# Kernel optimization log

Measured on AMD Instinct MI355X. Metric: run time of the kernel, lower is better.

## Reference

```python
import jax, jax.numpy as jnp
import numpy as np

S, B, H = 1024, 4, 1024
NH, NC = 16, 4            # num_attention_heads, num_combined_heads
HPH = H // NH             # 64
NF = NH // NC             # num_FFN = 4
FFM = 8                   # combined_FFN_multiple
DIN = NC * HPH            # 256, grouped FFN input dim
DHID = FFM * DIN          # 2048, dense_in output dim
DH2 = DHID // 2           # 1024, GLU half / dense_out input dim
EPS = 1e-6
NORM_FACTOR = 1.0 / float(np.sqrt(HPH))


def _ln(x, g, b):
    m = x.mean(-1, keepdims=True)
    v = ((x - m) ** 2).mean(-1, keepdims=True)
    return (x - m) * jax.lax.rsqrt(v + EPS) * g + b


def setup_inputs() -> dict:
    key = jax.random.key(0)
    ks = jax.random.split(key, 10)
    p = lambda k, shape: jax.random.normal(k, shape, jnp.float32) * 0.02
    return {
        "hidden_states": jax.random.normal(ks[0], (S, B, H), jnp.float32),
        "g1": jnp.ones((H,), jnp.float32), "b1": jnp.zeros((H,), jnp.float32),
        "g2": jnp.ones((HPH,), jnp.float32), "b2": jnp.zeros((HPH,), jnp.float32),
        "Wq": p(ks[1], (H, H)), "bq": jnp.zeros((H,), jnp.float32),
        "Wk": p(ks[2], (H, H)), "bk": jnp.zeros((H,), jnp.float32),
        "Wv": p(ks[3], (H, H)), "bv": jnp.zeros((H,), jnp.float32),
        "W_in": p(ks[4], (NF, DIN, DHID)), "b_in": jnp.zeros((NF, DHID), jnp.float32),
        "W_out": p(ks[5], (NF, DH2, DIN)), "b_out": jnp.zeros((NF, DIN), jnp.float32),
        "Wd": p(ks[6], (H, H)), "bd": jnp.zeros((H,), jnp.float32),
    }


def reference(hidden_states, g1, b1, g2, b2, Wq, bq, Wk, bk, Wv, bv,
              W_in, b_in, W_out, b_out, Wd, bd):
    # hidden_states: [S, B, H]
    x = _ln(hidden_states, g1, b1)                       # norm1

    def heads(t):  # [S,B,H] -> [B*NH, S, HPH] (matches view + transpose in torch)
        return jnp.transpose(t.reshape(S, B * NH, HPH), (1, 0, 2))

    q = heads(x @ Wq + bq)
    k = heads(x @ Wk + bk)
    v = heads(x @ Wv + bv)

    # subtraction_gaussian_kernel: pairwise squared euclidean distance
    qk = jnp.einsum('nsd,ntd->nst', q, k)                # [B*NH, S, S]
    q2 = jnp.sum(q * q, axis=-1)
    k2 = jnp.sum(k * k, axis=-1)
    dist = q2[:, :, None] + k2[None if False else slice(None), None, :][0] if False else q2[:, :, None] + k2[:, None, :] - 2.0 * qk
    matmul_result = dist * (-0.5 * NORM_FACTOR)          # scores <= 0

    # Exp sequence op: elementwise exp (softmax replacement, no normalization)
    probs = jnp.exp(matmul_result)

    ctx = jnp.einsum('nst,ntd->nsd', probs, v)           # [B*NH, S, HPH]
    ctx = jnp.transpose(ctx, (1, 0, 2)).reshape(S, B, H)
    ctx = x + ctx                                        # residual with norm1 output (as in source)

    ctx = _ln(ctx.reshape(S, B, NH, HPH), g2, b2)        # per-head norm2

    # grouped FFN over contiguous head subsets (vectorized over the NF groups)
    cg = ctx.reshape(S, B, NF, DIN)
    h = jnp.einsum('sbgi,gio->sbgo', cg, W_in) + b_in    # [S,B,NF,DHID]
    xh, yh = jnp.split(h, 2, axis=-1)
    h = xh * jax.nn.relu(yh)                             # GLU-style x * relu(y)
    og = jnp.einsum('sbgi,gio->sbgo', h, W_out) + b_out  # [S,B,NF,DIN]

    out = og.reshape(S, B, H) @ Wd + bd                  # attention_dense
    return out, matmul_result
```

## Files before the change

### kernel.cpp

```cpp
#include <hip/hip_runtime.h>


typedef __attribute__((ext_vector_type(8))) short short8;
typedef __attribute__((ext_vector_type(4))) float f32x4;

__device__ __forceinline__ unsigned short f2bf(float f) {
  union { float f; unsigned u; } x; x.f = f;
  unsigned r = x.u + 0x7FFFu + ((x.u >> 16) & 1u);
  return (unsigned short)(r >> 16);
}
__device__ __forceinline__ float bf2f(unsigned short u) {
  union { float f; unsigned u; } x; x.u = ((unsigned)u) << 16;
  return x.f;
}
__device__ __forceinline__ unsigned cvtpk(float a, float b) {
  unsigned r;
  asm("v_cvt_pk_bf16_f32 %0, %1, %2" : "=v"(r) : "v"(a), "v"(b));
  return r;
}
__device__ __forceinline__ void gload16(const unsigned short* g, unsigned short* l) {
  __builtin_amdgcn_global_load_lds(
      (const __attribute__((address_space(1))) unsigned int*)g,
      (__attribute__((address_space(3))) unsigned int*)l, 16, 0, 0);
}

__global__ __launch_bounds__(256) void ln1_kernel(
    const float* __restrict__ x, const float* __restrict__ g,
    const float* __restrict__ b, float* __restrict__ y,
    unsigned short* __restrict__ ybf)
{
  const long base = (long)blockIdx.x * 1024;
  const int c = threadIdx.x * 4;
  float4 v = *(const float4*)(x + base + c);
  float s = v.x + v.y + v.z + v.w;
  float ss = v.x*v.x + v.y*v.y + v.z*v.z + v.w*v.w;
  #pragma unroll
  for (int off = 32; off > 0; off >>= 1) {
    s  += __shfl_xor(s, off);
    ss += __shfl_xor(ss, off);
  }
  __shared__ float sw[4], ssw[4];
  const int wave = threadIdx.x >> 6;
  if ((threadIdx.x & 63) == 0) { sw[wave] = s; ssw[wave] = ss; }
  __syncthreads();
  s  = sw[0] + sw[1] + sw[2] + sw[3];
  ss = ssw[0] + ssw[1] + ssw[2] + ssw[3];
  const float mean = s * (1.0f/1024.0f);
  const float var  = ss * (1.0f/1024.0f) - mean*mean;
  const float rs   = rsqrtf(var + 1e-6f);
  const float4 gv = *(const float4*)(g + c);
  const float4 bv = *(const float4*)(b + c);
  float4 o;
  o.x = (v.x - mean) * rs * gv.x + bv.x;
  o.y = (v.y - mean) * rs * gv.y + bv.y;
  o.z = (v.z - mean) * rs * gv.z + bv.z;
  o.w = (v.w - mean) * rs * gv.w + bv.w;
  *(float4*)(y + base + c) = o;
  ushort4 ob;
  ob.x = f2bf(o.x); ob.y = f2bf(o.y); ob.z = f2bf(o.z); ob.w = f2bf(o.w);
  *(ushort4*)(ybf + base + c) = ob;
}

__device__ __forceinline__ void transpose_body(
    const float* __restrict__ Wg, unsigned short* __restrict__ WTg,
    int K, int N, int bx, int by, int tid)
{
  __shared__ float T[32][33];
  const int n0 = bx * 32, k0 = by * 32;
  const int r = tid >> 3, c4 = (tid & 7) * 4;
  float4 v = *(const float4*)(Wg + (long)(k0 + r) * N + n0 + c4);
  T[r][c4+0] = v.x; T[r][c4+1] = v.y; T[r][c4+2] = v.z; T[r][c4+3] = v.w;
  __syncthreads();
  ushort4 o;
  o.x = f2bf(T[c4+0][r]); o.y = f2bf(T[c4+1][r]);
  o.z = f2bf(T[c4+2][r]); o.w = f2bf(T[c4+3][r]);
  *(ushort4*)(WTg + (long)(n0 + r) * K + k0 + c4) = o;
}

__global__ __launch_bounds__(256) void prep_weights_kernel(
    const float* __restrict__ Wq, const float* __restrict__ Wk,
    const float* __restrict__ Wv, const float* __restrict__ Wd,
    const float* __restrict__ Win, const float* __restrict__ Wout,
    const float* __restrict__ bq, const float* __restrict__ bk,
    const float* __restrict__ bv,
    unsigned short* __restrict__ wqkvT, unsigned short* __restrict__ wdT,
    unsigned short* __restrict__ winT, unsigned short* __restrict__ woutT,
    float* __restrict__ qkvb)
{
  const int idx = blockIdx.x;
  const int tid = threadIdx.x;
  if (idx < 4096) {
    const int z = idx >> 10, rem = idx & 1023;
    const float* W = (z == 0) ? Wq : (z == 1) ? Wk : (z == 2) ? Wv : Wd;
    unsigned short* WT = (z == 3) ? wdT : wqkvT + (long)z * 1048576;
    transpose_body(W, WT, 1024, 1024, rem & 31, rem >> 5, tid);
  } else if (idx < 6144) {
    const int rem = idx - 4096;
    const int z = rem >> 9, r2 = rem & 511;
    transpose_body(Win + (long)z * 524288, winT + (long)z * 524288,
                   256, 2048, r2 & 63, r2 >> 6, tid);
  } else if (idx < 7168) {
    const int rem = idx - 6144;
    const int z = rem >> 8, r2 = rem & 255;
    transpose_body(Wout + (long)z * 262144, woutT + (long)z * 262144,
                   1024, 256, r2 & 7, r2 >> 3, tid);
  } else {
    const int i = (idx - 7168) * 256 + tid;
    qkvb[i] = (i < 1024) ? bq[i] : ((i < 2048) ? bk[i - 1024] : bv[i - 2048]);
  }
}

__global__ __launch_bounds__(256) void mfma_gemm_kernel(
    const unsigned short* __restrict__ A, int lda, long agoff,
    const unsigned short* __restrict__ BT, long bgoff, int K,
    const float* __restrict__ bias, int biasoff,
    unsigned short* __restrict__ Cbf, float* __restrict__ Cf,
    int ldc, int cgoff)
{
  const int g = blockIdx.z;
  const unsigned short* Ag = A + (long)g * agoff;
  const unsigned short* Bg = BT + (long)g * bgoff;
  const float* biasg = bias + (long)g * biasoff;
  const int row0 = blockIdx.y * 128, col0 = blockIdx.x * 128;
  __shared__ __align__(16) unsigned short As[128 * 64];
  __shared__ __align__(16) unsigned short Bs[128 * 64];
  const int tid = threadIdx.x;
  const int w = tid >> 6, l = tid & 63;
  const int ms = (w & 1) << 6, ns = (w >> 1) << 6;
  const int fr = l & 15, fg = l >> 4;
  const int lr8 = l >> 3, ls8 = l & 7;
  const int scol = (ls8 ^ lr8) << 3;
  const int rsw = fr & 7;
  f32x4 acc[4][4];
  #pragma unroll
  for (int i = 0; i < 4; ++i)
    #pragma unroll
    for (int j = 0; j < 4; ++j) acc[i][j] = (f32x4)0.0f;

  for (int k0 = 0; k0 < K; k0 += 64) {
    #pragma unroll
    for (int g8 = 0; g8 < 4; ++g8) {
      const int r = (w << 5) + (g8 << 3);
      gload16(Ag + (long)(row0 + r + lr8) * lda + k0 + scol, &As[r * 64]);
      gload16(Bg + (long)(col0 + r + lr8) * K  + k0 + scol, &Bs[r * 64]);
    }
    __syncthreads();
    #pragma unroll
    for (int ks = 0; ks < 2; ++ks) {
      const int rslot = (((ks << 2) + fg) ^ rsw) << 3;
      short8 af[4], bfr[4];
      #pragma unroll
      for (int i = 0; i < 4; ++i)
        af[i] = *(const short8*)&As[(ms + i*16 + fr) * 64 + rslot];
      #pragma unroll
      for (int j = 0; j < 4; ++j)
        bfr[j] = *(const short8*)&Bs[(ns + j*16 + fr) * 64 + rslot];
      #pragma unroll
      for (int i = 0; i < 4; ++i)
        #pragma unroll
        for (int j = 0; j < 4; ++j)
          acc[i][j] = __builtin_amdgcn_mfma_f32_16x16x32_bf16(bfr[j], af[i], acc[i][j], 0, 0, 0);
    }
    __syncthreads();
  }

  #pragma unroll
  for (int j = 0; j < 4; ++j) {
    const float4 bj4 = *(const float4*)(biasg + col0 + ns + j*16 + (fg << 2));
    #pragma unroll
    for (int i = 0; i < 4; ++i) {
      const long row = row0 + ms + i*16 + fr;
      const long cb = row * ldc + (long)g * cgoff + col0 + ns + j*16 + (fg << 2);
      const float v0 = acc[i][j][0] + bj4.x, v1 = acc[i][j][1] + bj4.y;
      const float v2 = acc[i][j][2] + bj4.z, v3 = acc[i][j][3] + bj4.w;
      if (Cbf) {
        uint2 pk; pk.x = cvtpk(v0, v1); pk.y = cvtpk(v2, v3);
        *(uint2*)(Cbf + cb) = pk;
      } else {
        f32x4 o = {v0, v1, v2, v3};
        __builtin_nontemporal_store(o, (f32x4*)(Cf + cb));
      }
    }
  }
}

__global__ __launch_bounds__(256) void mfma_gemm64_kernel(
    const unsigned short* __restrict__ A, int lda, long agoff,
    const unsigned short* __restrict__ BT, long bgoff, int K,
    const float* __restrict__ bias, int biasoff,
    unsigned short* __restrict__ Cbf, float* __restrict__ Cf,
    int ldc, int cgoff)
{
  const int g = blockIdx.z;
  const unsigned short* Ag = A + (long)g * agoff;
  const unsigned short* Bg = BT + (long)g * bgoff;
  const float* biasg = bias + (long)g * biasoff;
  const int row0 = blockIdx.y * 128, col0 = blockIdx.x * 64;
  __shared__ __align__(16) unsigned short As[128 * 64];
  __shared__ __align__(16) unsigned short Bs[64 * 64];
  const int tid = threadIdx.x;
  const int w = tid >> 6, l = tid & 63;
  const int ms = (w & 1) << 6, ns = (w >> 1) << 5;
  const int fr = l & 15, fg = l >> 4;
  const int lr8 = l >> 3, ls8 = l & 7;
  const int scol = (ls8 ^ lr8) << 3;
  const int rsw = fr & 7;
  f32x4 acc[4][2];
  #pragma unroll
  for (int i = 0; i < 4; ++i)
    #pragma unroll
    for (int j = 0; j < 2; ++j) acc[i][j] = (f32x4)0.0f;

  for (int k0 = 0; k0 < K; k0 += 64) {
    #pragma unroll
    for (int g8 = 0; g8 < 4; ++g8) {
      const int r = (w << 5) + (g8 << 3);
      gload16(Ag + (long)(row0 + r + lr8) * lda + k0 + scol, &As[r * 64]);
    }
    #pragma unroll
    for (int g8 = 0; g8 < 2; ++g8) {
      const int r = (w << 4) + (g8 << 3);
      gload16(Bg + (long)(col0 + r + lr8) * K + k0 + scol, &Bs[r * 64]);
    }
    __syncthreads();
    #pragma unroll
    for (int ks = 0; ks < 2; ++ks) {
      const int rslot = (((ks << 2) + fg) ^ rsw) << 3;
      short8 af[4], bfr[2];
      #pragma unroll
      for (int i = 0; i < 4; ++i)
        af[i] = *(const short8*)&As[(ms + i*16 + fr) * 64 + rslot];
      #pragma unroll
      for (int j = 0; j < 2; ++j)
        bfr[j] = *(const short8*)&Bs[(ns + j*16 + fr) * 64 + rslot];
      #pragma unroll
      for (int i = 0; i < 4; ++i)
        #pragma unroll
        for (int j = 0; j < 2; ++j)
          acc[i][j] = __builtin_amdgcn_mfma_f32_16x16x32_bf16(bfr[j], af[i], acc[i][j], 0, 0, 0);
    }
    __syncthreads();
  }

  #pragma unroll
  for (int j = 0; j < 2; ++j) {
    const float4 bj4 = *(const float4*)(biasg + col0 + ns + j*16 + (fg << 2));
    #pragma unroll
    for (int i = 0; i < 4; ++i) {
      const long row = row0 + ms + i*16 + fr;
      const long cb = row * ldc + (long)g * cgoff + col0 + ns + j*16 + (fg << 2);
      const float v0 = acc[i][j][0] + bj4.x, v1 = acc[i][j][1] + bj4.y;
      const float v2 = acc[i][j][2] + bj4.z, v3 = acc[i][j][3] + bj4.w;
      if (Cbf) {
        uint2 pk; pk.x = cvtpk(v0, v1); pk.y = cvtpk(v2, v3);
        *(uint2*)(Cbf + cb) = pk;
      } else {
        f32x4 o = {v0, v1, v2, v3};
        __builtin_nontemporal_store(o, (f32x4*)(Cf + cb));
      }
    }
  }
}

__global__ __launch_bounds__(256) void mfma_glu_kernel(
    const unsigned short* __restrict__ A,
    const unsigned short* __restrict__ WT,
    const float* __restrict__ bin,
    unsigned short* __restrict__ H2)
{
  const int g = blockIdx.z;
  const unsigned short* Ag = A + g * 256;
  const unsigned short* Wg = WT + (long)g * 2048 * 256;
  const float* bg = bin + g * 2048;
  const int row0 = blockIdx.y * 128, col0 = blockIdx.x * 64;
  __shared__ __align__(16) unsigned short As[128 * 64];
  __shared__ __align__(16) unsigned short Bxs[64 * 64];
  __shared__ __align__(16) unsigned short Bys[64 * 64];
  const int tid = threadIdx.x;
  const int w = tid >> 6, l = tid & 63;
  const int ms = (w & 1) << 6, ns = (w >> 1) << 5;
  const int fr = l & 15, fg = l >> 4;
  const int lr8 = l >> 3, ls8 = l & 7;
  const int scol = (ls8 ^ lr8) << 3;
  const int rsw = fr & 7;
  f32x4 ax[4][2], ay[4][2];
  #pragma unroll
  for (int i = 0; i < 4; ++i)
    #pragma unroll
    for (int j = 0; j < 2; ++j) { ax[i][j] = (f32x4)0.0f; ay[i][j] = (f32x4)0.0f; }

  for (int k0 = 0; k0 < 256; k0 += 64) {
    #pragma unroll
    for (int g8 = 0; g8 < 4; ++g8) {
      const int r = (w << 5) + (g8 << 3);
      gload16(Ag + (long)(row0 + r + lr8) * 1024 + k0 + scol, &As[r * 64]);
    }
    #pragma unroll
    for (int g8 = 0; g8 < 2; ++g8) {
      const int r = (w << 4) + (g8 << 3);
      gload16(Wg + (long)(col0 + r + lr8) * 256 + k0 + scol,          &Bxs[r * 64]);
      gload16(Wg + (long)(1024 + col0 + r + lr8) * 256 + k0 + scol,   &Bys[r * 64]);
    }
    __syncthreads();
    #pragma unroll
    for (int ks = 0; ks < 2; ++ks) {
      const int rslot = (((ks << 2) + fg) ^ rsw) << 3;
      short8 af[4], bx[2], by[2];
      #pragma unroll
      for (int i = 0; i < 4; ++i)
        af[i] = *(const short8*)&As[(ms + i*16 + fr) * 64 + rslot];
      #pragma unroll
      for (int j = 0; j < 2; ++j) {
        bx[j] = *(const short8*)&Bxs[(ns + j*16 + fr) * 64 + rslot];
        by[j] = *(const short8*)&Bys[(ns + j*16 + fr) * 64 + rslot];
      }
      #pragma unroll
      for (int i = 0; i < 4; ++i)
        #pragma unroll
        for (int j = 0; j < 2; ++j) {
          ax[i][j] = __builtin_amdgcn_mfma_f32_16x16x32_bf16(bx[j], af[i], ax[i][j], 0, 0, 0);
          ay[i][j] = __builtin_amdgcn_mfma_f32_16x16x32_bf16(by[j], af[i], ay[i][j], 0, 0, 0);
        }
    }
    __syncthreads();
  }

  #pragma unroll
  for (int j = 0; j < 2; ++j) {
    const float4 bx4 = *(const float4*)(bg + col0 + ns + j*16 + (fg << 2));
    const float4 by4 = *(const float4*)(bg + 1024 + col0 + ns + j*16 + (fg << 2));
    #pragma unroll
    for (int i = 0; i < 4; ++i) {
      const long row = row0 + ms + i*16 + fr;
      const long cb = row * 4096 + g * 1024 + col0 + ns + j*16 + (fg << 2);
      float o4[4];
      const float* bxp = &bx4.x; const float* byp = &by4.x;
      #pragma unroll
      for (int r4 = 0; r4 < 4; ++r4) {
        const float xh = ax[i][j][r4] + bxp[r4];
        const float yh = ay[i][j][r4] + byp[r4];
        o4[r4] = xh * fmaxf(yh, 0.0f);
      }
      uint2 pk; pk.x = cvtpk(o4[0], o4[1]); pk.y = cvtpk(o4[2], o4[3]);
      *(uint2*)(H2 + cb) = pk;
    }
  }
}

__global__ __launch_bounds__(256) void prep_attn_kernel(
    const unsigned short* __restrict__ qkv,
    float* __restrict__ q2g, float* __restrict__ k2g,
    unsigned short* __restrict__ vt)
{
  const int n = blockIdx.y, s0 = blockIdx.x * 64;
  const int b = n >> 4, hoff = (n & 15) * 64;
  const int tid = threadIdx.x;
  __shared__ unsigned short T[64][72];
  #pragma unroll
  for (int p = 0; p < 2; ++p) {
    const int r = (tid >> 3) + p * 32, c = (tid & 7) << 3;
    *(short8*)&T[r][c] = *(const short8*)(qkv + ((long)((s0 + r) * 4 + b)) * 3072 + 2048 + hoff + c);
  }
  {
    const int r = tid >> 2, e = tid & 3;
    const long base = ((long)((s0 + r) * 4 + b)) * 3072 + hoff + (e << 4);
    float sq = 0.f, sk = 0.f;
    #pragma unroll
    for (int ch = 0; ch < 2; ++ch) {
      short8 q8 = *(const short8*)(qkv + base + (ch << 3));
      short8 k8 = *(const short8*)(qkv + base + 1024 + (ch << 3));
      #pragma unroll
      for (int ee = 0; ee < 8; ++ee) {
        float f = bf2f((unsigned short)q8[ee]); sq = fmaf(f, f, sq);
        f = bf2f((unsigned short)k8[ee]); sk = fmaf(f, f, sk);
      }
    }
    sq += __shfl_xor(sq, 1); sq += __shfl_xor(sq, 2);
    sk += __shfl_xor(sk, 1); sk += __shfl_xor(sk, 2);
    if (e == 0) {
      q2g[n * 1024 + s0 + r] = sq;
      k2g[n * 1024 + s0 + r] = sk;
    }
  }
  __syncthreads();
  #pragma unroll
  for (int p = 0; p < 2; ++p) {
    const int d = (tid >> 3) + p * 32, sc = (tid & 7) << 3;
    short8 o;
    #pragma unroll
    for (int j = 0; j < 8; ++j) o[j] = (short)T[sc + j][d];
    *(short8*)(vt + ((long)n * 64 + d) * 1024 + s0 + sc) = o;
  }
}

__global__ __launch_bounds__(256) void attn_kernel(
    const unsigned short* __restrict__ qkv, const unsigned short* __restrict__ vt,
    const float* __restrict__ q2g, const float* __restrict__ k2g,
    const float* __restrict__ xln, const float* __restrict__ g2,
    const float* __restrict__ b2,
    unsigned short* __restrict__ ctx2, float* __restrict__ scores)
{
  const int n = blockIdx.y;
  const int s0 = blockIdx.x * 64;
  const int b = n >> 4, hoff = (n & 15) * 64;
  __shared__ __align__(16) unsigned short Qs[64][72];
  __shared__ __align__(16) unsigned short Ks[2][64 * 64];
  __shared__ __align__(16) unsigned short VTl[2][64 * 64];
  __shared__ __align__(16) unsigned short Ps[64][72];
  const int tid = threadIdx.x, w = tid >> 6, l = tid & 63;
  const int fr = l & 15, fg = l >> 4;
  const int lr8 = l >> 3, ls8 = l & 7;
  const int sslot = ((ls8 ^ lr8) << 3);
  const int rsw = fr & 7;

  #pragma unroll
  for (int p = 0; p < 2; ++p) {
    const int r = (tid >> 3) + p * 32, c = (tid & 7) << 3;
    *(short8*)&Qs[r][c] = *(const short8*)(qkv + ((long)((s0 + r) * 4 + b)) * 3072 + hoff + c);
  }
  float q2m[4];
  #pragma unroll
  for (int i = 0; i < 4; ++i) q2m[i] = -0.0625f * q2g[n * 1024 + s0 + i*16 + fr];

  #pragma unroll
  for (int p = 0; p < 2; ++p) {
    const int rowb = p * 32 + w * 8;
    gload16(qkv + ((long)((rowb + lr8) * 4 + b)) * 3072 + 1024 + hoff + sslot, &Ks[0][rowb * 64]);
    gload16(vt + ((long)n * 64 + rowb + lr8) * 1024 + sslot,                   &VTl[0][rowb * 64]);
  }
  __syncthreads();

  f32x4 o[4];
  #pragma unroll
  for (int i = 0; i < 4; ++i) o[i] = (f32x4)0.0f;

  int cur = 0;
  for (int t0 = 0; t0 < 1024; t0 += 64) {
    if (t0 + 64 < 1024) {
      #pragma unroll
      for (int p = 0; p < 2; ++p) {
        const int rowb = p * 32 + w * 8;
        gload16(qkv + ((long)((t0 + 64 + rowb + lr8) * 4 + b)) * 3072 + 1024 + hoff + sslot,
                &Ks[cur ^ 1][rowb * 64]);
        gload16(vt + ((long)n * 64 + rowb + lr8) * 1024 + t0 + 64 + sslot,
                &VTl[cur ^ 1][rowb * 64]);
      }
    }
    const float4 k2v4 = *(const float4*)(k2g + n * 1024 + t0 + (w << 4) + (fg << 2));
    const float k2m[4] = {-0.0625f*k2v4.x, -0.0625f*k2v4.y, -0.0625f*k2v4.z, -0.0625f*k2v4.w};

    f32x4 c4[4];
    #pragma unroll
    for (int i = 0; i < 4; ++i) c4[i] = (f32x4)0.0f;
    #pragma unroll
    for (int ks = 0; ks < 2; ++ks) {
      const short8 kf = *(const short8*)&Ks[cur][((w << 4) + fr) * 64 + ((((ks << 2) + fg) ^ rsw) << 3)];
      #pragma unroll
      for (int i = 0; i < 4; ++i) {
        const short8 qf = *(const short8*)&Qs[i*16 + fr][(ks << 5) + (fg << 3)];
        c4[i] = __builtin_amdgcn_mfma_f32_16x16x32_bf16(kf, qf, c4[i], 0, 0, 0);
      }
    }
    #pragma unroll
    for (int i = 0; i < 4; ++i) {
      f32x4 sc;
      float pe[4];
      #pragma unroll
      for (int r4 = 0; r4 < 4; ++r4) {
        const float m = fmaf(c4[i][r4], 0.125f, q2m[i] + k2m[r4]);
        sc[r4] = m;
        pe[r4] = __expf(m);
      }
      __builtin_nontemporal_store(sc,
          (f32x4*)(scores + (long)n * 1048576 + (long)(s0 + i*16 + fr) * 1024 + t0 + (w << 4) + (fg << 2)));
      uint2 pk; pk.x = cvtpk(pe[0], pe[1]); pk.y = cvtpk(pe[2], pe[3]);
      *(uint2*)&Ps[i*16 + fr][(w << 4) + (fg << 2)] = pk;
    }
    __syncthreads();

    #pragma unroll
    for (int ks = 0; ks < 2; ++ks) {
      const short8 vb = *(const short8*)&VTl[cur][((w << 4) + fr) * 64 + ((((ks << 2) + fg) ^ rsw) << 3)];
      #pragma unroll
      for (int i = 0; i < 4; ++i) {
        const short8 pf = *(const short8*)&Ps[i*16 + fr][(ks << 5) + (fg << 3)];
        o[i] = __builtin_amdgcn_mfma_f32_16x16x32_bf16(vb, pf, o[i], 0, 0, 0);
      }
    }
    __syncthreads();
    cur ^= 1;
  }

  const int dbase = (w << 4) + (fg << 2);
  float4 xl4[4];
  #pragma unroll
  for (int i = 0; i < 4; ++i)
    xl4[i] = *(const float4*)(xln + ((long)((s0 + i*16 + fr) * 4 + b)) * 1024 + hoff + dbase);

  float* redbuf = (float*)&Ps[0][0];
  const int slot = (w << 2) + fg;
  #pragma unroll
  for (int i = 0; i < 4; ++i) {
    float s = 0.f, ss = 0.f;
    const float* xp = &xl4[i].x;
    #pragma unroll
    for (int r4 = 0; r4 < 4; ++r4) {
      const float v = o[i][r4] + xp[r4];
      s += v; ss = fmaf(v, v, ss);
    }
    redbuf[(i*16 + fr) * 16 + slot] = s;
    redbuf[1024 + (i*16 + fr) * 16 + slot] = ss;
  }
  __syncthreads();
  float* statbuf = (float*)&Qs[0][0];
  {
    const int row = tid >> 2, q4 = tid & 3;
    float s = 0.f, ss = 0.f;
    #pragma unroll
    for (int k = 0; k < 4; ++k) {
      s  += redbuf[row * 16 + q4 * 4 + k];
      ss += redbuf[1024 + row * 16 + q4 * 4 + k];
    }
    s  += __shfl_xor(s, 1);  s  += __shfl_xor(s, 2);
    ss += __shfl_xor(ss, 1); ss += __shfl_xor(ss, 2);
    if (q4 == 0) {
      const float mean = s * (1.0f/64.0f);
      const float var  = ss * (1.0f/64.0f) - mean * mean;
      statbuf[row] = mean;
      statbuf[64 + row] = rsqrtf(var + 1e-6f);
    }
  }
  __syncthreads();
  const float4 g2v = *(const float4*)(g2 + dbase);
  const float4 b2v = *(const float4*)(b2 + dbase);
  const float* gp = &g2v.x; const float* bp = &b2v.x;
  #pragma unroll
  for (int i = 0; i < 4; ++i) {
    const float mean = statbuf[i*16 + fr];
    const float rs   = statbuf[64 + i*16 + fr];
    const float* xp = &xl4[i].x;
    float vo[4];
    #pragma unroll
    for (int r4 = 0; r4 < 4; ++r4)
      vo[r4] = (o[i][r4] + xp[r4] - mean) * rs * gp[r4] + bp[r4];
    uint2 pk; pk.x = cvtpk(vo[0], vo[1]); pk.y = cvtpk(vo[2], vo[3]);
    *(uint2*)(ctx2 + ((long)((s0 + i*16 + fr) * 4 + b)) * 1024 + hoff + dbase) = pk;
  }
}

extern "C" void kernel_launch(void* const* d_in, const int* in_sizes, int n_in,
                              void* d_out, int out_size, void* d_ws, size_t ws_size,
                              hipStream_t stream) {
  const float* hs   = (const float*)d_in[0];
  const float* g1   = (const float*)d_in[1];
  const float* b1   = (const float*)d_in[2];
  const float* g2   = (const float*)d_in[3];
  const float* b2   = (const float*)d_in[4];
  const float* Wq   = (const float*)d_in[5];
  const float* bq   = (const float*)d_in[6];
  const float* Wk   = (const float*)d_in[7];
  const float* bk   = (const float*)d_in[8];
  const float* Wv   = (const float*)d_in[9];
  const float* bv   = (const float*)d_in[10];
  const float* Win  = (const float*)d_in[11];
  const float* bin  = (const float*)d_in[12];
  const float* Wout = (const float*)d_in[13];
  const float* bout = (const float*)d_in[14];
  const float* Wd   = (const float*)d_in[15];
  const float* bd   = (const float*)d_in[16];

  char* ws = (char*)d_ws;
  float*          xln   = (float*)(ws + 0);
  unsigned short* xbf   = (unsigned short*)(ws + 16777216);
  unsigned short* qkv   = (unsigned short*)(ws + 25165824);
  unsigned short* ctx2  = (unsigned short*)(ws + 67108864);
  unsigned short* wqkvT = (unsigned short*)(ws + 75497472);
  unsigned short* winT  = (unsigned short*)(ws + 81788928);
  unsigned short* woutT = (unsigned short*)(ws + 85983232);
  unsigned short* wdT   = (unsigned short*)(ws + 88080384);
  float*          qkvb  = (float*)(ws + 90177536);
  unsigned short* vt    = (unsigned short*)(ws + 90189824);
  float*          q2g   = (float*)(ws + 98578432);
  float*          k2g   = (float*)(ws + 98840576);
  unsigned short* h2    = (unsigned short*)(ws + 16777216);
  unsigned short* og    = (unsigned short*)(ws + 0);

  float* out0 = (float*)d_out;
  float* out1 = out0 + 4194304;

  ln1_kernel<<<4096, 256, 0, stream>>>(hs, g1, b1, xln, xbf);

  prep_weights_kernel<<<7180, 256, 0, stream>>>(
      Wq, Wk, Wv, Wd, Win, Wout, bq, bk, bv, wqkvT, wdT, winT, woutT, qkvb);

  mfma_gemm_kernel<<<dim3(24,32,1), 256, 0, stream>>>(
      xbf, 1024, 0, wqkvT, 0, 1024, qkvb, 0, qkv, nullptr, 3072, 0);

  prep_attn_kernel<<<dim3(16,64), 256, 0, stream>>>(qkv, q2g, k2g, vt);

  attn_kernel<<<dim3(16,64), 256, 0, stream>>>(qkv, vt, q2g, k2g, xln, g2, b2, ctx2, out1);

  mfma_glu_kernel<<<dim3(16,32,4), 256, 0, stream>>>(ctx2, winT, bin, h2);

  mfma_gemm64_kernel<<<dim3(4,32,4), 256, 0, stream>>>(
      h2, 4096, 1024, woutT, 262144, 1024, bout, 256, og, nullptr, 1024, 256);

  mfma_gemm64_kernel<<<dim3(16,32,1), 256, 0, stream>>>(
      og, 1024, 0, wdT, 0, 1024, bd, 0, nullptr, out0, 1024, 0);
}
```

Baseline: 246.5 us.

## Double-buffer LDS tiles with async prefetch in MFMA GEMM kernels

The three MFMA GEMM kernels (generic 128x128, 128x64, and GLU) now keep two LDS stages. Global-to-LDS loads for tile t+2 are issued right after the fragments of tile t have been read into registers, with explicit vmcnt waits, barriers and raised priority around the MFMA block. This is meant to overlap global memory latency with matrix compute instead of stalling on every K step. In exchange it doubles LDS use, which may lower occupancy, and it relies on hand-counted vmcnt values that must match the number of loads in flight.

```diff
diff --git a/kernel.cpp b/kernel.cpp
--- a/kernel.cpp
+++ b/kernel.cpp
@@ -122,8 +122,8 @@
   const unsigned short* Bg = BT + (long)g * bgoff;
   const float* biasg = bias + (long)g * biasoff;
   const int row0 = blockIdx.y * 128, col0 = blockIdx.x * 128;
-  __shared__ __align__(16) unsigned short As[128 * 64];
-  __shared__ __align__(16) unsigned short Bs[128 * 64];
+  __shared__ __align__(16) unsigned short As[2][128 * 64];
+  __shared__ __align__(16) unsigned short Bs[2][128 * 64];
   const int tid = threadIdx.x;
   const int w = tid >> 6, l = tid & 63;
   const int ms = (w & 1) << 6, ns = (w >> 1) << 6;
@@ -137,31 +137,55 @@
     #pragma unroll
     for (int j = 0; j < 4; ++j) acc[i][j] = (f32x4)0.0f;
 
-  for (int k0 = 0; k0 < K; k0 += 64) {
+  const int nt = K >> 6;
+  #pragma unroll
+  for (int sidx = 0; sidx < 2; ++sidx) {
+    const int k0 = sidx << 6;
     #pragma unroll
     for (int g8 = 0; g8 < 4; ++g8) {
       const int r = (w << 5) + (g8 << 3);
-      gload16(Ag + (long)(row0 + r + lr8) * lda + k0 + scol, &As[r * 64]);
-      gload16(Bg + (long)(col0 + r + lr8) * K  + k0 + scol, &Bs[r * 64]);
-    }
-    __syncthreads();
+      gload16(Ag + (long)(row0 + r + lr8) * lda + k0 + scol, &As[sidx][r * 64]);
+      gload16(Bg + (long)(col0 + r + lr8) * K  + k0 + scol, &Bs[sidx][r * 64]);
+    }
+  }
+  int cur = 0;
+  for (int t = 0; t < nt; ++t) {
+    if (t + 1 < nt) asm volatile("s_waitcnt vmcnt(8)" ::: "memory");
+    else            asm volatile("s_waitcnt vmcnt(0)" ::: "memory");
+    __builtin_amdgcn_s_barrier();
+    __builtin_amdgcn_sched_barrier(0);
+    short8 af[2][4], bfr[2][4];
     #pragma unroll
     for (int ks = 0; ks < 2; ++ks) {
       const int rslot = (((ks << 2) + fg) ^ rsw) << 3;
-      short8 af[4], bfr[4];
-      #pragma unroll
-      for (int i = 0; i < 4; ++i)
-        af[i] = *(const short8*)&As[(ms + i*16 + fr) * 64 + rslot];
-      #pragma unroll
-      for (int j = 0; j < 4; ++j)
-        bfr[j] = *(const short8*)&Bs[(ns + j*16 + fr) * 64 + rslot];
+      #pragma unroll
+      for (int i = 0; i < 4; ++i) {
+        af[ks][i]  = *(const short8*)&As[cur][(ms + i*16 + fr) * 64 + rslot];
+        bfr[ks][i] = *(const short8*)&Bs[cur][(ns + i*16 + fr) * 64 + rslot];
+      }
+    }
+    asm volatile("s_waitcnt lgkmcnt(0)" ::: "memory");
+    __builtin_amdgcn_sched_barrier(0);
+    __builtin_amdgcn_s_barrier();
+    if (t + 2 < nt) {
+      const int k0 = (t + 2) << 6;
+      #pragma unroll
+      for (int g8 = 0; g8 < 4; ++g8) {
+        const int r = (w << 5) + (g8 << 3);
+        gload16(Ag + (long)(row0 + r + lr8) * lda + k0 + scol, &As[cur][r * 64]);
+        gload16(Bg + (long)(col0 + r + lr8) * K  + k0 + scol, &Bs[cur][r * 64]);
+      }
+    }
+    __builtin_amdgcn_s_setprio(1);
+    #pragma unroll
+    for (int ks = 0; ks < 2; ++ks)
       #pragma unroll
       for (int i = 0; i < 4; ++i)
         #pragma unroll
         for (int j = 0; j < 4; ++j)
-          acc[i][j] = __builtin_amdgcn_mfma_f32_16x16x32_bf16(bfr[j], af[i], acc[i][j], 0, 0, 0);
-    }
-    __syncthreads();
+          acc[i][j] = __builtin_amdgcn_mfma_f32_16x16x32_bf16(bfr[ks][j], af[ks][i], acc[i][j], 0, 0, 0);
+    __builtin_amdgcn_s_setprio(0);
+    cur ^= 1;
   }
 
   #pragma unroll
@@ -196,8 +220,8 @@
   const unsigned short* Bg = BT + (long)g * bgoff;
   const float* biasg = bias + (long)g * biasoff;
   const int row0 = blockIdx.y * 128, col0 = blockIdx.x * 64;
-  __shared__ __align__(16) unsigned short As[128 * 64];
-  __shared__ __align__(16) unsigned short Bs[64 * 64];
+  __shared__ __align__(16) unsigned short As[2][128 * 64];
+  __shared__ __align__(16) unsigned short Bs[2][64 * 64];
   const int tid = threadIdx.x;
   const int w = tid >> 6, l = tid & 63;
   const int ms = (w & 1) << 6, ns = (w >> 1) << 5;
@@ -211,35 +235,64 @@
     #pragma unroll
     for (int j = 0; j < 2; ++j) acc[i][j] = (f32x4)0.0f;
 
-  for (int k0 = 0; k0 < K; k0 += 64) {
+  const int nt = K >> 6;
+  #pragma unroll
+  for (int sidx = 0; sidx < 2; ++sidx) {
+    const int k0 = sidx << 6;
     #pragma unroll
     for (int g8 = 0; g8 < 4; ++g8) {
       const int r = (w << 5) + (g8 << 3);
-      gload16(Ag + (long)(row0 + r + lr8) * lda + k0 + scol, &As[r * 64]);
+      gload16(Ag + (long)(row0 + r + lr8) * lda + k0 + scol, &As[sidx][r * 64]);
     }
     #pragma unroll
     for (int g8 = 0; g8 < 2; ++g8) {
       const int r = (w << 4) + (g8 << 3);
-      gload16(Bg + (long)(col0 + r + lr8) * K + k0 + scol, &Bs[r * 64]);
-    }
-    __syncthreads();
+      gload16(Bg + (long)(col0 + r + lr8) * K + k0 + scol, &Bs[sidx][r * 64]);
+    }
+  }
+  int cur = 0;
+  for (int t = 0; t < nt; ++t) {
+    if (t + 1 < nt) asm volatile("s_waitcnt vmcnt(6)" ::: "memory");
+    else            asm volatile("s_waitcnt vmcnt(0)" ::: "memory");
+    __builtin_amdgcn_s_barrier();
+    __builtin_amdgcn_sched_barrier(0);
+    short8 af[2][4], bfr[2][2];
     #pragma unroll
     for (int ks = 0; ks < 2; ++ks) {
       const int rslot = (((ks << 2) + fg) ^ rsw) << 3;
-      short8 af[4], bfr[2];
       #pragma unroll
       for (int i = 0; i < 4; ++i)
-        af[i] = *(const short8*)&As[(ms + i*16 + fr) * 64 + rslot];
+        af[ks][i] = *(const short8*)&As[cur][(ms + i*16 + fr) * 64 + rslot];
       #pragma unroll
       for (int j = 0; j < 2; ++j)
-        bfr[j] = *(const short8*)&Bs[(ns + j*16 + fr) * 64 + rslot];
+        bfr[ks][j] = *(const short8*)&Bs[cur][(ns + j*16 + fr) * 64 + rslot];
+    }
+    asm volatile("s_waitcnt lgkmcnt(0)" ::: "memory");
+    __builtin_amdgcn_sched_barrier(0);
+    __builtin_amdgcn_s_barrier();
+    if (t + 2 < nt) {
+      const int k0 = (t + 2) << 6;
+      #pragma unroll
+      for (int g8 = 0; g8 < 4; ++g8) {
+        const int r = (w << 5) + (g8 << 3);
+        gload16(Ag + (long)(row0 + r + lr8) * lda + k0 + scol, &As[cur][r * 64]);
+      }
+      #pragma unroll
+      for (int g8 = 0; g8 < 2; ++g8) {
+        const int r = (w << 4) + (g8 << 3);
+        gload16(Bg + (long)(col0 + r + lr8) * K + k0 + scol, &Bs[cur][r * 64]);
+      }
+    }
+    __builtin_amdgcn_s_setprio(1);
+    #pragma unroll
+    for (int ks = 0; ks < 2; ++ks)
       #pragma unroll
       for (int i = 0; i < 4; ++i)
         #pragma unroll
         for (int j = 0; j < 2; ++j)
-          acc[i][j] = __builtin_amdgcn_mfma_f32_16x16x32_bf16(bfr[j], af[i], acc[i][j], 0, 0, 0);
-    }
-    __syncthreads();
+          acc[i][j] = __builtin_amdgcn_mfma_f32_16x16x32_bf16(bfr[ks][j], af[ks][i], acc[i][j], 0, 0, 0);
+    __builtin_amdgcn_s_setprio(0);
+    cur ^= 1;
   }
 
   #pragma unroll
@@ -273,9 +326,9 @@
   const unsigned short* Wg = WT + (long)g * 2048 * 256;
   const float* bg = bin + g * 2048;
   const int row0 = blockIdx.y * 128, col0 = blockIdx.x * 64;
-  __shared__ __align__(16) unsigned short As[128 * 64];
-  __shared__ __align__(16) unsigned short Bxs[64 * 64];
-  __shared__ __align__(16) unsigned short Bys[64 * 64];
+  __shared__ __align__(16) unsigned short As[2][128 * 64];
+  __shared__ __align__(16) unsigned short Bxs[2][64 * 64];
+  __shared__ __align__(16) unsigned short Bys[2][64 * 64];
   const int tid = threadIdx.x;
   const int w = tid >> 6, l = tid & 63;
   const int ms = (w & 1) << 6, ns = (w >> 1) << 5;
@@ -289,40 +342,69 @@
     #pragma unroll
     for (int j = 0; j < 2; ++j) { ax[i][j] = (f32x4)0.0f; ay[i][j] = (f32x4)0.0f; }
 
-  for (int k0 = 0; k0 < 256; k0 += 64) {
+  #pragma unroll
+  for (int sidx = 0; sidx < 2; ++sidx) {
+    const int k0 = sidx << 6;
     #pragma unroll
     for (int g8 = 0; g8 < 4; ++g8) {
       const int r = (w << 5) + (g8 << 3);
-      gload16(Ag + (long)(row0 + r + lr8) * 1024 + k0 + scol, &As[r * 64]);
+      gload16(Ag + (long)(row0 + r + lr8) * 1024 + k0 + scol, &As[sidx][r * 64]);
     }
     #pragma unroll
     for (int g8 = 0; g8 < 2; ++g8) {
       const int r = (w << 4) + (g8 << 3);
-      gload16(Wg + (long)(col0 + r + lr8) * 256 + k0 + scol,          &Bxs[r * 64]);
-      gload16(Wg + (long)(1024 + col0 + r + lr8) * 256 + k0 + scol,   &Bys[r * 64]);
-    }
-    __syncthreads();
+      gload16(Wg + (long)(col0 + r + lr8) * 256 + k0 + scol,        &Bxs[sidx][r * 64]);
+      gload16(Wg + (long)(1024 + col0 + r + lr8) * 256 + k0 + scol, &Bys[sidx][r * 64]);
+    }
+  }
+  int cur = 0;
+  for (int t = 0; t < 4; ++t) {
+    if (t + 1 < 4) asm volatile("s_waitcnt vmcnt(8)" ::: "memory");
+    else           asm volatile("s_waitcnt vmcnt(0)" ::: "memory");
+    __builtin_amdgcn_s_barrier();
+    __builtin_amdgcn_sched_barrier(0);
+    short8 af[2][4], bx[2][2], by[2][2];
     #pragma unroll
     for (int ks = 0; ks < 2; ++ks) {
       const int rslot = (((ks << 2) + fg) ^ rsw) << 3;
-      short8 af[4], bx[2], by[2];
       #pragma unroll
       for (int i = 0; i < 4; ++i)
-        af[i] = *(const short8*)&As[(ms + i*16 + fr) * 64 + rslot];
+        af[ks][i] = *(const short8*)&As[cur][(ms + i*16 + fr) * 64 + rslot];
       #pragma unroll
       for (int j = 0; j < 2; ++j) {
-        bx[j] = *(const short8*)&Bxs[(ns + j*16 + fr) * 64 + rslot];
-        by[j] = *(const short8*)&Bys[(ns + j*16 + fr) * 64 + rslot];
-      }
+        bx[ks][j] = *(const short8*)&Bxs[cur][(ns + j*16 + fr) * 64 + rslot];
+        by[ks][j] = *(const short8*)&Bys[cur][(ns + j*16 + fr) * 64 + rslot];
+      }
+    }
+    asm volatile("s_waitcnt lgkmcnt(0)" ::: "memory");
+    __builtin_amdgcn_sched_barrier(0);
+    __builtin_amdgcn_s_barrier();
+    if (t + 2 < 4) {
+      const int k0 = (t + 2) << 6;
+      #pragma unroll
+      for (int g8 = 0; g8 < 4; ++g8) {
+        const int r = (w << 5) + (g8 << 3);
+        gload16(Ag + (long)(row0 + r + lr8) * 1024 + k0 + scol, &As[cur][r * 64]);
+      }
+      #pragma unroll
+      for (int g8 = 0; g8 < 2; ++g8) {
+        const int r = (w << 4) + (g8 << 3);
+        gload16(Wg + (long)(col0 + r + lr8) * 256 + k0 + scol,        &Bxs[cur][r * 64]);
+        gload16(Wg + (long)(1024 + col0 + r + lr8) * 256 + k0 + scol, &Bys[cur][r * 64]);
+      }
+    }
+    __builtin_amdgcn_s_setprio(1);
+    #pragma unroll
+    for (int ks = 0; ks < 2; ++ks)
       #pragma unroll
       for (int i = 0; i < 4; ++i)
         #pragma unroll
         for (int j = 0; j < 2; ++j) {
-          ax[i][j] = __builtin_amdgcn_mfma_f32_16x16x32_bf16(bx[j], af[i], ax[i][j], 0, 0, 0);
-          ay[i][j] = __builtin_amdgcn_mfma_f32_16x16x32_bf16(by[j], af[i], ay[i][j], 0, 0, 0);
+          ax[i][j] = __builtin_amdgcn_mfma_f32_16x16x32_bf16(bx[ks][j], af[ks][i], ax[i][j], 0, 0, 0);
+          ay[i][j] = __builtin_amdgcn_mfma_f32_16x16x32_bf16(by[ks][j], af[ks][i], ay[i][j], 0, 0, 0);
         }
-    }
-    __syncthreads();
+    __builtin_amdgcn_s_setprio(0);
+    cur ^= 1;
   }
 
   #pragma unroll
```

Result: no change. 243.8 us (-1.1%).
